# Performance work log

Hardware: AMD Instinct MI355X
Metric: run time of the kernel (lower is better)

## Reference

```python
import jax, jax.numpy as jnp
import numpy as np

B, T, D, H = 256, 512, 128, 64


def _gru_dir(x_tbd, Wi, Wh, bi, bh):
    # PyTorch GRU semantics. x_tbd: [T,B,D]; Wi: [3H,D]; Wh: [3H,H].
    xg = jnp.einsum('tbd,gd->tbg', x_tbd, Wi) + bi  # [T,B,3H]

    def step(h, xg_t):
        hg = h @ Wh.T + bh
        xr, xz, xn = jnp.split(xg_t, 3, axis=-1)
        hr, hz, hn = jnp.split(hg, 3, axis=-1)
        r = jax.nn.sigmoid(xr + hr)
        z = jax.nn.sigmoid(xz + hz)
        n = jnp.tanh(xn + r * hn)
        h = (1.0 - z) * n + z * h
        return h, h

    h0 = jnp.zeros((x_tbd.shape[1], Wh.shape[1]), x_tbd.dtype)
    _, hs = jax.lax.scan(step, h0, xg)
    return hs  # [T,B,H]


def _hb_dir(x_tbd, W, b, U, c):
    # Custom HBLSTM cell. W: [D,5H] (input proj), U: [H,5H] (hidden proj).
    # Gate order: f, i, o, u, k. Both biases folded into the x projection.
    xp = jnp.einsum('tbd,dg->tbg', x_tbd, W) + b + c  # [T,B,5H]

    def step(carry, xp_t):
        h, k, kp = carry
        pre = xp_t + h @ U
        f, i, o, u, kc = jnp.split(pre, 5, axis=-1)
        f = jax.nn.sigmoid(f)
        i = jax.nn.sigmoid(i)
        o = jax.nn.sigmoid(o)
        u = jax.nn.sigmoid(u)
        kp = u * jnp.tanh(kc) + (1.0 - u) * kp
        k = f * k + i * kp
        h = o * jnp.tanh(k)
        return (h, k, kp), h

    z = jnp.zeros((x_tbd.shape[1], U.shape[0]), x_tbd.dtype)
    _, hs = jax.lax.scan(step, (z, z, z), xp)
    return hs  # [T,B,H]


def _forward(x, gru_f_Wi, gru_f_Wh, gru_f_bi, gru_f_bh,
             gru_b_Wi, gru_b_Wh, gru_b_bi, gru_b_bh,
             hb_f_W, hb_f_b, hb_f_U, hb_f_c,
             hb_b_W, hb_b_b, hb_b_U, hb_b_c,
             fast_W, fast_b, stab_W, stab_b,
             attnp_W, attnp_b, attns_W, attns_b,
             gate_W1, gate_b1, gate_W2, gate_b2,
             head_W1, head_b1, head_W2, head_b2):
    xt = jnp.transpose(x, (1, 0, 2))  # [T,B,D]
    xr = xt[::-1]

    # Fast branch: bidirectional GRU; only last-timestep output is used.
    hf = _gru_dir(xt, gru_f_Wi, gru_f_Wh, gru_f_bi, gru_f_bh)
    hb_ = _gru_dir(xr, gru_b_Wi, gru_b_Wh, gru_b_bi, gru_b_bh)
    # fast_seq[:, -1, :] = [fwd hidden at t=T-1, bwd hidden at t=T-1]
    fast_last = jnp.concatenate([hf[-1], hb_[0]], axis=-1) @ fast_W + fast_b

    # Stable branch: bidirectional HBLSTM.
    sf = _hb_dir(xt, hb_f_W, hb_f_b, hb_f_U, hb_f_c)
    sb = _hb_dir(xr, hb_b_W, hb_b_b, hb_b_U, hb_b_c)[::-1]
    stable_seq = jnp.transpose(jnp.concatenate([sf, sb], axis=-1), (1, 0, 2))  # [B,T,2H]

    # Attention pooling over time.
    attn_hidden = jnp.tanh(stable_seq @ attnp_W + attnp_b)        # [B,T,H]
    logits = (attn_hidden @ attns_W + attns_b)[..., 0]            # [B,T]
    w = jax.nn.softmax(logits, axis=1)
    stable_ctx = jnp.einsum('bt,btd->bd', w, stable_seq)
    stable_ctx = stable_ctx @ stab_W + stab_b                     # [B,2H]

    # Gated fusion (dropout is identity in eval).
    g_in = jnp.concatenate([fast_last, stable_ctx], axis=-1)      # [B,4H]
    g_h = jax.nn.relu(g_in @ gate_W1 + gate_b1)
    gate = jax.nn.sigmoid(g_h @ gate_W2 + gate_b2)                # [B,1]
    fused = gate * fast_last + (1.0 - gate) * stable_ctx

    out = jnp.concatenate([fused, fast_last, stable_ctx], axis=-1)  # [B,6H]
    h1 = jax.nn.relu(out @ head_W1 + head_b1)
    return h1 @ head_W2 + head_b2                                  # [B,1]


def setup_inputs() -> dict:
    key = jax.random.key(0)
    ks = iter(jax.random.split(key, 64))

    def p(shape, fan_in):
        return jax.random.normal(next(ks), shape, dtype=jnp.float32) / np.sqrt(fan_in)

    d = {'x': jax.random.normal(next(ks), (B, T, D), dtype=jnp.float32)}
    for pre in ('gru_f', 'gru_b'):
        d[pre + '_Wi'] = p((3 * H, D), D)
        d[pre + '_Wh'] = p((3 * H, H), H)
        d[pre + '_bi'] = p((3 * H,), H)
        d[pre + '_bh'] = p((3 * H,), H)
    for pre in ('hb_f', 'hb_b'):
        d[pre + '_W'] = p((D, 5 * H), D)
        d[pre + '_b'] = p((5 * H,), D)
        d[pre + '_U'] = p((H, 5 * H), H)
        d[pre + '_c'] = p((5 * H,), H)
    d['fast_W'] = p((2 * H, 2 * H), 2 * H); d['fast_b'] = p((2 * H,), 2 * H)
    d['stab_W'] = p((2 * H, 2 * H), 2 * H); d['stab_b'] = p((2 * H,), 2 * H)
    d['attnp_W'] = p((2 * H, H), 2 * H);   d['attnp_b'] = p((H,), 2 * H)
    d['attns_W'] = p((H, 1), H);           d['attns_b'] = p((1,), H)
    d['gate_W1'] = p((4 * H, 2 * H), 4 * H); d['gate_b1'] = p((2 * H,), 4 * H)
    d['gate_W2'] = p((2 * H, 1), 2 * H);     d['gate_b2'] = p((1,), 2 * H)
    d['head_W1'] = p((6 * H, 2 * H), 6 * H); d['head_b1'] = p((2 * H,), 6 * H)
    d['head_W2'] = p((2 * H, 1), 2 * H);     d['head_b2'] = p((1,), 2 * H)
    return d


def reference(x, gru_f_Wi, gru_f_Wh, gru_f_bi, gru_f_bh,
              gru_b_Wi, gru_b_Wh, gru_b_bi, gru_b_bh,
              hb_f_W, hb_f_b, hb_f_U, hb_f_c,
              hb_b_W, hb_b_b, hb_b_U, hb_b_c,
              fast_W, fast_b, stab_W, stab_b,
              attnp_W, attnp_b, attns_W, attns_b,
              gate_W1, gate_b1, gate_W2, gate_b2,
              head_W1, head_b1, head_W2, head_b2):
    return _forward(x, gru_f_Wi, gru_f_Wh, gru_f_bi, gru_f_bh,
                    gru_b_Wi, gru_b_Wh, gru_b_bi, gru_b_bh,
                    hb_f_W, hb_f_b, hb_f_U, hb_f_c,
                    hb_b_W, hb_b_b, hb_b_U, hb_b_c,
                    fast_W, fast_b, stab_W, stab_b,
                    attnp_W, attnp_b, attns_W, attns_b,
                    gate_W1, gate_b1, gate_W2, gate_b2,
                    head_W1, head_b1, head_W2, head_b2)
```

## Files before the change

### kernel.cpp

```cpp
#include <hip/hip_runtime.h>
#include <math.h>

#define B_ 256
#define T_ 512
#define D_ 128
#define H_ 64

static const size_t F_SF    = 0;
static const size_t F_SB    = F_SF + (size_t)T_ * B_ * 64;
static const size_t F_ST    = F_SB + (size_t)T_ * B_ * 64;
static const size_t F_FASTL = F_ST + (size_t)7 * B_ * 64;
static const size_t F_LOG   = F_FASTL + (size_t)B_ * 128;
static const size_t F_CTX   = F_LOG + (size_t)B_ * T_;
static const size_t F_CHUNK = F_CTX + (size_t)B_ * 128;

__device__ __forceinline__ float sigmoidf_(float x) {
    return 1.0f / (1.0f + __expf(-x));
}
__device__ __forceinline__ float tanhf_(float x) {
    float ax = fabsf(x);
    float e  = __expf(-2.0f * ax);
    float t  = (1.0f - e) / (1.0f + e);
    return copysignf(t, x);
}
__device__ __forceinline__ float rl_(float v, int lane) {
    return __int_as_float(__builtin_amdgcn_readlane(__float_as_int(v), lane));
}
__device__ __forceinline__ float wave_sum(float v) {
#pragma unroll
    for (int off = 32; off > 0; off >>= 1) v += __shfl_xor(v, off);
    return v;
}
__device__ __forceinline__ float wave_max(float v) {
#pragma unroll
    for (int off = 32; off > 0; off >>= 1) v = fmaxf(v, __shfl_xor(v, off));
    return v;
}

template<int N, bool WGD, bool REV>
__global__ __launch_bounds__(256) void gemm_in(
    const float* __restrict__ x, const float* __restrict__ W,
    const float* __restrict__ b1, const float* __restrict__ b2,
    float* __restrict__ out, int t0)
{
    __shared__ float a_lds[64 * 68];
    __shared__ float w_lds[64 * 68];

    const int tid = threadIdx.x;
    const int tl  = blockIdx.z;
    const int tg  = t0 + tl;
    const int txi = REV ? (T_ - 1 - tg) : tg;
    const int b0  = blockIdx.y * 64;
    const int g0  = blockIdx.x * 64;

    const int ty = tid >> 4, tx = tid & 15;
    float acc[4][4] = {};

    for (int kh = 0; kh < 2; kh++) {
#pragma unroll
        for (int i = 0; i < 4; i++) {
            int flat = i * 256 + tid;
            int r  = flat >> 4;
            int c4 = flat & 15;
            const float4 v = *reinterpret_cast<const float4*>(
                x + ((size_t)(b0 + r) * T_ + txi) * D_ + kh * 64 + c4 * 4);
            a_lds[(c4 * 4 + 0) * 68 + r] = v.x;
            a_lds[(c4 * 4 + 1) * 68 + r] = v.y;
            a_lds[(c4 * 4 + 2) * 68 + r] = v.z;
            a_lds[(c4 * 4 + 3) * 68 + r] = v.w;
        }
        if (WGD) {
#pragma unroll
            for (int i = 0; i < 4; i++) {
                int flat = i * 256 + tid;
                int r  = flat >> 4;
                int c4 = flat & 15;
                const float4 v = *reinterpret_cast<const float4*>(
                    W + (size_t)(g0 + r) * D_ + kh * 64 + c4 * 4);
                w_lds[(c4 * 4 + 0) * 68 + r] = v.x;
                w_lds[(c4 * 4 + 1) * 68 + r] = v.y;
                w_lds[(c4 * 4 + 2) * 68 + r] = v.z;
                w_lds[(c4 * 4 + 3) * 68 + r] = v.w;
            }
        } else {
#pragma unroll
            for (int i = 0; i < 4; i++) {
                int flat = i * 256 + tid;
                int k  = flat >> 4;
                int c4 = flat & 15;
                const float4 v = *reinterpret_cast<const float4*>(
                    W + (size_t)(kh * 64 + k) * N + g0 + c4 * 4);
                *reinterpret_cast<float4*>(&w_lds[k * 68 + c4 * 4]) = v;
            }
        }
        __syncthreads();
#pragma unroll 8
        for (int k = 0; k < 64; k++) {
            const float4 av = *reinterpret_cast<const float4*>(&a_lds[k * 68 + ty * 4]);
            const float4 wv = *reinterpret_cast<const float4*>(&w_lds[k * 68 + tx * 4]);
            const float am[4] = {av.x, av.y, av.z, av.w};
            const float wn[4] = {wv.x, wv.y, wv.z, wv.w};
#pragma unroll
            for (int mi = 0; mi < 4; mi++)
#pragma unroll
                for (int ni = 0; ni < 4; ni++)
                    acc[mi][ni] = fmaf(am[mi], wn[ni], acc[mi][ni]);
        }
        __syncthreads();
    }

    float bias[4];
#pragma unroll
    for (int ni = 0; ni < 4; ni++) {
        float bb = b1[g0 + tx * 4 + ni];
        if (b2 != nullptr) bb += b2[g0 + tx * 4 + ni];
        bias[ni] = bb;
    }
#pragma unroll
    for (int mi = 0; mi < 4; mi++) {
        float4 o;
        o.x = acc[mi][0] + bias[0];
        o.y = acc[mi][1] + bias[1];
        o.z = acc[mi][2] + bias[2];
        o.w = acc[mi][3] + bias[3];
        *reinterpret_cast<float4*>(
            out + ((size_t)tl * B_ + b0 + ty * 4 + mi) * N + g0 + tx * 4) = o;
    }
}

__global__ __launch_bounds__(256, 1) void recur(
    const float* __restrict__ xg_c, const float* __restrict__ xpf_c,
    const float* __restrict__ xpb_c,
    const float* __restrict__ gWh, const float* __restrict__ gbh,
    const float* __restrict__ Uf,  const float* __restrict__ Ub,
    float* __restrict__ sf, float* __restrict__ sb,
    float* __restrict__ state, int t0, int C)
{
    const int tid   = threadIdx.x;
    const int w     = tid & 63;
    const int wb    = tid >> 6;
    const int chain = blockIdx.x * 4 + wb;

    if (chain < 256) {
        const int batch = chain;
        float* stH = state;
        float h = (t0 == 0) ? 0.0f : stH[(size_t)batch * 64 + w];

        float wh0[64], wh1[64], wh2[64];
#pragma unroll
        for (int j = 0; j < 64; j++) {
            wh0[j] = gWh[(size_t)(0 * 64 + w) * 64 + j];
            wh1[j] = gWh[(size_t)(1 * 64 + w) * 64 + j];
            wh2[j] = gWh[(size_t)(2 * 64 + w) * 64 + j];
            asm volatile("" : "+v"(wh0[j]), "+v"(wh1[j]), "+v"(wh2[j]));
        }
        const float bh0 = gbh[w], bh1 = gbh[64 + w], bh2 = gbh[128 + w];

        float xv0, xv1, xv2;
        {
            const float* p = xg_c + (size_t)batch * 192;
            xv0 = p[w]; xv1 = p[64 + w]; xv2 = p[128 + w];
        }
        for (int t = 0; t < C; t++) {
            float xn0, xn1, xn2;
            {
                int tn = (t + 1 < C) ? (t + 1) : t;
                const float* pn = xg_c + ((size_t)tn * B_ + batch) * 192;
                xn0 = pn[w]; xn1 = pn[64 + w]; xn2 = pn[128 + w];
            }
            float a0 = bh0, a1 = bh1, a2 = bh2;
#pragma unroll
            for (int j = 0; j < 64; j++) {
                const float hj = rl_(h, j);
                a0 = fmaf(hj, wh0[j], a0);
                a1 = fmaf(hj, wh1[j], a1);
                a2 = fmaf(hj, wh2[j], a2);
            }
            float r = sigmoidf_(xv0 + a0);
            float z = sigmoidf_(xv1 + a1);
            float n = tanhf_(xv2 + r * a2);
            h = (1.0f - z) * n + z * h;
            xv0 = xn0; xv1 = xn1; xv2 = xn2;
        }
        stH[(size_t)batch * 64 + w] = h;
    } else {
        const int dir   = (chain >= 512);
        const int batch = chain - (dir ? 512 : 256);
        const float* U  = dir ? Ub : Uf;
        const float* xp = dir ? xpb_c : xpf_c;
        float* outbuf   = dir ? sb : sf;
        float* stH  = state + (size_t)(1 + dir * 3) * B_ * 64;
        float* stK  = stH + (size_t)B_ * 64;
        float* stKp = stK + (size_t)B_ * 64;

        float h, k, kp;
        if (t0 == 0) { h = 0.0f; k = 0.0f; kp = 0.0f; }
        else {
            h  = stH [(size_t)batch * 64 + w];
            k  = stK [(size_t)batch * 64 + w];
            kp = stKp[(size_t)batch * 64 + w];
        }

        float u0[64], u1[64], u2[64], u3[64], u4[64];
#pragma unroll
        for (int j = 0; j < 64; j++) {
            const float* Uj = U + (size_t)j * 320 + w;
            u0[j] = Uj[0];
            u1[j] = Uj[64];
            u2[j] = Uj[128];
            u3[j] = Uj[192];
            u4[j] = Uj[256];
            asm volatile("" : "+v"(u0[j]), "+v"(u1[j]), "+v"(u2[j]),
                              "+v"(u3[j]), "+v"(u4[j]));
        }

        float xv0, xv1, xv2, xv3, xv4;
        {
            const float* p = xp + (size_t)batch * 320;
            xv0 = p[w]; xv1 = p[64 + w]; xv2 = p[128 + w];
            xv3 = p[192 + w]; xv4 = p[256 + w];
        }
        for (int t = 0; t < C; t++) {
            float xn0, xn1, xn2, xn3, xn4;
            {
                int tn = (t + 1 < C) ? (t + 1) : t;
                const float* pn = xp + ((size_t)tn * B_ + batch) * 320;
                xn0 = pn[w]; xn1 = pn[64 + w]; xn2 = pn[128 + w];
                xn3 = pn[192 + w]; xn4 = pn[256 + w];
            }
            float a0 = 0.f, a1 = 0.f, a2 = 0.f, a3 = 0.f, a4 = 0.f;
#pragma unroll
            for (int j = 0; j < 64; j++) {
                const float hj = rl_(h, j);
                a0 = fmaf(hj, u0[j], a0);
                a1 = fmaf(hj, u1[j], a1);
                a2 = fmaf(hj, u2[j], a2);
                a3 = fmaf(hj, u3[j], a3);
                a4 = fmaf(hj, u4[j], a4);
            }
            float f   = sigmoidf_(xv0 + a0);
            float ii  = sigmoidf_(xv1 + a1);
            float o   = sigmoidf_(xv2 + a2);
            float uu  = sigmoidf_(xv3 + a3);
            float tkc = tanhf_(xv4 + a4);
            kp = uu * tkc + (1.0f - uu) * kp;
            k  = f * k + ii * kp;
            h  = o * tanhf_(k);
            int tg   = t0 + t;
            int tout = dir ? (T_ - 1 - tg) : tg;
            outbuf[((size_t)tout * B_ + batch) * 64 + w] = h;
            xv0 = xn0; xv1 = xn1; xv2 = xn2; xv3 = xn3; xv4 = xn4;
        }
        stH [(size_t)batch * 64 + w] = h;
        stK [(size_t)batch * 64 + w] = k;
        stKp[(size_t)batch * 64 + w] = kp;
    }
}

__global__ __launch_bounds__(64) void tail1(
    const float* __restrict__ x, const float* __restrict__ Wib,
    const float* __restrict__ bib, const float* __restrict__ bhb,
    const float* __restrict__ hfl, const float* __restrict__ fW,
    const float* __restrict__ fb, float* __restrict__ fastl)
{
    __shared__ float xrow[128];
    __shared__ float inb[128];
    const int b = blockIdx.x;
    const int l = threadIdx.x;
    xrow[l]      = x[((size_t)b * T_ + (T_ - 1)) * D_ + l];
    xrow[64 + l] = x[((size_t)b * T_ + (T_ - 1)) * D_ + 64 + l];
    inb[l] = hfl[(size_t)b * 64 + l];
    __syncthreads();
    float a0 = bib[l], a1 = bib[64 + l], a2 = bib[128 + l];
#pragma unroll 8
    for (int d = 0; d < 128; d++) {
        float xd = xrow[d];
        a0 = fmaf(xd, Wib[(size_t)l * 128 + d], a0);
        a1 = fmaf(xd, Wib[(size_t)(64 + l) * 128 + d], a1);
        a2 = fmaf(xd, Wib[(size_t)(128 + l) * 128 + d], a2);
    }
    float r = sigmoidf_(a0 + bhb[l]);
    float z = sigmoidf_(a1 + bhb[64 + l]);
    float n = tanhf_(a2 + r * bhb[128 + l]);
    inb[64 + l] = (1.0f - z) * n;
    __syncthreads();
    float acc0 = fb[l], acc1 = fb[64 + l];
#pragma unroll 8
    for (int i2 = 0; i2 < 128; i2++) {
        float v = inb[i2];
        acc0 = fmaf(v, fW[(size_t)i2 * 128 + l], acc0);
        acc1 = fmaf(v, fW[(size_t)i2 * 128 + 64 + l], acc1);
    }
    fastl[(size_t)b * 128 + l]      = acc0;
    fastl[(size_t)b * 128 + 64 + l] = acc1;
}

__global__ __launch_bounds__(256) void attn_logits(
    const float* __restrict__ sf, const float* __restrict__ sb,
    const float* __restrict__ Wp, const float* __restrict__ bp,
    const float* __restrict__ Ws, const float* __restrict__ bs,
    float* __restrict__ logits)
{
    __shared__ float wp_t[64 * 129];
    __shared__ float s_lds[4][132];
    __shared__ float bp_l[64], ws_l[64];
    const int tid = threadIdx.x;
#pragma unroll
    for (int i = 0; i < 32; i++) {
        int idx = i * 256 + tid;
        int d = idx >> 6, g = idx & 63;
        wp_t[g * 129 + d] = Wp[idx];
    }
    if (tid < 64) { bp_l[tid] = bp[tid]; ws_l[tid] = Ws[tid]; }
    __syncthreads();
    const int wave = tid >> 6, l = tid & 63;
    for (int it = 0; it < 64; it++) {
        int p  = blockIdx.x * 256 + wave * 64 + it;
        int bb = p >> 9;
        int t  = p & 511;
        s_lds[wave][l]      = sf[((size_t)t * B_ + bb) * 64 + l];
        s_lds[wave][64 + l] = sb[((size_t)t * B_ + bb) * 64 + l];
        float acc = bp_l[l];
#pragma unroll 8
        for (int d = 0; d < 128; d++)
            acc = fmaf(s_lds[wave][d], wp_t[l * 129 + d], acc);
        float v = tanhf_(acc) * ws_l[l];
        v = wave_sum(v);
        if (l == 0) logits[(size_t)bb * T_ + t] = v + bs[0];
    }
}

__global__ __launch_bounds__(256) void softmax_k(float* __restrict__ logits)
{
    __shared__ float red[8];
    const int b = blockIdx.x, tid = threadIdx.x;
    const int wave = tid >> 6, l = tid & 63;
    float* row = logits + (size_t)b * T_;
    float l0 = row[tid], l1 = row[tid + 256];
    float m = wave_max(fmaxf(l0, l1));
    if (l == 0) red[wave] = m;
    __syncthreads();
    m = fmaxf(fmaxf(red[0], red[1]), fmaxf(red[2], red[3]));
    float e0 = __expf(l0 - m), e1 = __expf(l1 - m);
    float s = wave_sum(e0 + e1);
    if (l == 0) red[4 + wave] = s;
    __syncthreads();
    s = red[4] + red[5] + red[6] + red[7];
    row[tid]       = e0 / s;
    row[tid + 256] = e1 / s;
}

__global__ __launch_bounds__(128) void ctx_k(
    const float* __restrict__ wsm, const float* __restrict__ sf,
    const float* __restrict__ sb, const float* __restrict__ stW,
    const float* __restrict__ stb, float* __restrict__ ctxo)
{
    __shared__ float wrow[512];
    __shared__ float cpre[128];
    const int b = blockIdx.x, tid = threadIdx.x;
#pragma unroll
    for (int i = 0; i < 4; i++) wrow[i * 128 + tid] = wsm[(size_t)b * T_ + i * 128 + tid];
    __syncthreads();
    const float* src = (tid < 64) ? sf : sb;
    const int d = tid & 63;
    float acc = 0.0f;
#pragma unroll 4
    for (int t = 0; t < 512; t++)
        acc = fmaf(wrow[t], src[((size_t)t * B_ + b) * 64 + d], acc);
    cpre[tid] = acc;
    __syncthreads();
    float a2 = stb[tid];
#pragma unroll 8
    for (int i2 = 0; i2 < 128; i2++)
        a2 = fmaf(cpre[i2], stW[(size_t)i2 * 128 + tid], a2);
    ctxo[(size_t)b * 128 + tid] = a2;
}

__global__ __launch_bounds__(128) void tail2(
    const float* __restrict__ fastl, const float* __restrict__ ctxo,
    const float* __restrict__ gW1, const float* __restrict__ gb1,
    const float* __restrict__ gW2, const float* __restrict__ gb2,
    const float* __restrict__ hW1, const float* __restrict__ hb1,
    const float* __restrict__ hW2, const float* __restrict__ hb2,
    float* __restrict__ outp)
{
    __shared__ float gin[256];
    __shared__ float outv[384];
    __shared__ float red2[2];
    const int b = blockIdx.x, tid = threadIdx.x;
    gin[tid]       = fastl[(size_t)b * 128 + tid];
    gin[128 + tid] = ctxo[(size_t)b * 128 + tid];
    __syncthreads();
    float a = gb1[tid];
#pragma unroll 8
    for (int i = 0; i < 256; i++)
        a = fmaf(gin[i], gW1[(size_t)i * 128 + tid], a);
    float gh = fmaxf(a, 0.0f);
    float v = wave_sum(gh * gW2[tid]);
    if ((tid & 63) == 0) red2[tid >> 6] = v;
    __syncthreads();
    float gate = sigmoidf_(red2[0] + red2[1] + gb2[0]);
    float fl = gin[tid], sc = gin[128 + tid];
    outv[tid]       = gate * fl + (1.0f - gate) * sc;
    outv[128 + tid] = fl;
    outv[256 + tid] = sc;
    __syncthreads();
    float a1 = hb1[tid];
#pragma unroll 8
    for (int i = 0; i < 384; i++)
        a1 = fmaf(outv[i], hW1[(size_t)i * 128 + tid], a1);
    float h1v = fmaxf(a1, 0.0f);
    float vv = wave_sum(h1v * hW2[tid]);
    if ((tid & 63) == 0) red2[tid >> 6] = vv;
    __syncthreads();
    if (tid == 0) outp[b] = red2[0] + red2[1] + hb2[0];
}

extern "C" void kernel_launch(void* const* d_in, const int* in_sizes, int n_in,
                              void* d_out, int out_size, void* d_ws, size_t ws_size,
                              hipStream_t stream)
{
    (void)in_sizes; (void)n_in; (void)out_size;
    const float* x      = (const float*)d_in[0];
    const float* gfWi   = (const float*)d_in[1];
    const float* gfWh   = (const float*)d_in[2];
    const float* gfbi   = (const float*)d_in[3];
    const float* gfbh   = (const float*)d_in[4];
    const float* gbWi   = (const float*)d_in[5];
    const float* gbbi   = (const float*)d_in[7];
    const float* gbbh   = (const float*)d_in[8];
    const float* hbfW   = (const float*)d_in[9];
    const float* hbfb   = (const float*)d_in[10];
    const float* hbfU   = (const float*)d_in[11];
    const float* hbfc   = (const float*)d_in[12];
    const float* hbbW   = (const float*)d_in[13];
    const float* hbbb   = (const float*)d_in[14];
    const float* hbbU   = (const float*)d_in[15];
    const float* hbbc   = (const float*)d_in[16];
    const float* fastW  = (const float*)d_in[17];
    const float* fastb  = (const float*)d_in[18];
    const float* stabW  = (const float*)d_in[19];
    const float* stabb  = (const float*)d_in[20];
    const float* attnpW = (const float*)d_in[21];
    const float* attnpb = (const float*)d_in[22];
    const float* attnsW = (const float*)d_in[23];
    const float* attnsb = (const float*)d_in[24];
    const float* gW1    = (const float*)d_in[25];
    const float* gb1    = (const float*)d_in[26];
    const float* gW2    = (const float*)d_in[27];
    const float* gb2    = (const float*)d_in[28];
    const float* hW1    = (const float*)d_in[29];
    const float* hb1    = (const float*)d_in[30];
    const float* hW2    = (const float*)d_in[31];
    const float* hb2    = (const float*)d_in[32];

    float* ws    = (float*)d_ws;
    float* sf    = ws + F_SF;
    float* sb    = ws + F_SB;
    float* st    = ws + F_ST;
    float* fastl = ws + F_FASTL;
    float* logit = ws + F_LOG;
    float* ctxo  = ws + F_CTX;

    const size_t wsf = ws_size / sizeof(float);
    int C = T_;
    while (C > 1 && F_CHUNK + (size_t)C * B_ * 832 > wsf) C >>= 1;
    const int nc = T_ / C;

    float* xg_c  = ws + F_CHUNK;
    float* xpf_c = xg_c  + (size_t)C * B_ * 192;
    float* xpb_c = xpf_c + (size_t)C * B_ * 320;

    for (int c = 0; c < nc; c++) {
        const int t0 = c * C;
        gemm_in<192, true,  false><<<dim3(3, 4, C), 256, 0, stream>>>(x, gfWi, gfbi, nullptr, xg_c, t0);
        gemm_in<320, false, false><<<dim3(5, 4, C), 256, 0, stream>>>(x, hbfW, hbfb, hbfc, xpf_c, t0);
        gemm_in<320, false, true ><<<dim3(5, 4, C), 256, 0, stream>>>(x, hbbW, hbbb, hbbc, xpb_c, t0);
        recur<<<dim3(192), 256, 0, stream>>>(xg_c, xpf_c, xpb_c, gfWh, gfbh, hbfU, hbbU,
                                             sf, sb, st, t0, C);
    }

    tail1<<<dim3(B_), 64, 0, stream>>>(x, gbWi, gbbi, gbbh, st, fastW, fastb, fastl);

    attn_logits<<<dim3(512), 256, 0, stream>>>(sf, sb, attnpW, attnpb, attnsW, attnsb, logit);
    softmax_k<<<dim3(B_), 256, 0, stream>>>(logit);
    ctx_k<<<dim3(B_), 128, 0, stream>>>(logit, sf, sb, stabW, stabb, ctxo);

    tail2<<<dim3(B_), 128, 0, stream>>>(fastl, ctxo, gW1, gb1, gW2, gb2,
                                        hW1, hb1, hW2, hb2, (float*)d_out);
}
```

Baseline: 1.598 ms.

## Split recurrent matvec across two waves per chain and enlarge input GEMM tiles

The recurrent kernel now splits each chain's hidden-state matvec across two wavefronts. Each wave holds half of the recurrent weights and exchanges partial sums through double-buffered LDS with a block barrier every timestep. This halves the serial FMA chain per step and the register pressure, at the cost of a __syncthreads per timestep that couples the chains sharing a block. Separately, the input-projection GEMM tile grows to 128 batch rows with 8x4 accumulators per thread and XOR-swizzled LDS addressing to reduce bank conflicts.

```diff
diff --git a/kernel.cpp b/kernel.cpp
--- a/kernel.cpp
+++ b/kernel.cpp
@@ -37,71 +37,110 @@
     return v;
 }
 
+template<int BASE>
+__device__ __forceinline__ void hb_acc(float h,
+    const float* u0, const float* u1, const float* u2,
+    const float* u3, const float* u4,
+    float& a0, float& a1, float& a2, float& a3, float& a4)
+{
+#pragma unroll
+    for (int jj = 0; jj < 32; jj++) {
+        const float hj = rl_(h, BASE + jj);
+        a0 = fmaf(hj, u0[jj], a0);
+        a1 = fmaf(hj, u1[jj], a1);
+        a2 = fmaf(hj, u2[jj], a2);
+        a3 = fmaf(hj, u3[jj], a3);
+        a4 = fmaf(hj, u4[jj], a4);
+    }
+}
+template<int BASE>
+__device__ __forceinline__ void gru_acc(float h,
+    const float* w0, const float* w1, const float* w2,
+    float& a0, float& a1, float& a2)
+{
+#pragma unroll
+    for (int jj = 0; jj < 32; jj++) {
+        const float hj = rl_(h, BASE + jj);
+        a0 = fmaf(hj, w0[jj], a0);
+        a1 = fmaf(hj, w1[jj], a1);
+        a2 = fmaf(hj, w2[jj], a2);
+    }
+}
+
 template<int N, bool WGD, bool REV>
-__global__ __launch_bounds__(256) void gemm_in(
+__global__ __launch_bounds__(256, 1) void gemm_in(
     const float* __restrict__ x, const float* __restrict__ W,
     const float* __restrict__ b1, const float* __restrict__ b2,
     float* __restrict__ out, int t0)
 {
-    __shared__ float a_lds[64 * 68];
+    __shared__ float a_lds[64 * 132];
     __shared__ float w_lds[64 * 68];
 
     const int tid = threadIdx.x;
     const int tl  = blockIdx.z;
     const int tg  = t0 + tl;
     const int txi = REV ? (T_ - 1 - tg) : tg;
-    const int b0  = blockIdx.y * 64;
+    const int b0  = blockIdx.y * 128;
     const int g0  = blockIdx.x * 64;
 
     const int ty = tid >> 4, tx = tid & 15;
-    float acc[4][4] = {};
+    float acc[8][4] = {};
 
     for (int kh = 0; kh < 2; kh++) {
 #pragma unroll
-        for (int i = 0; i < 4; i++) {
+        for (int i = 0; i < 8; i++) {
             int flat = i * 256 + tid;
-            int r  = flat >> 4;
-            int c4 = flat & 15;
+            int r    = flat >> 4;
+            int c4   = flat & 15;
             const float4 v = *reinterpret_cast<const float4*>(
                 x + ((size_t)(b0 + r) * T_ + txi) * D_ + kh * 64 + c4 * 4);
-            a_lds[(c4 * 4 + 0) * 68 + r] = v.x;
-            a_lds[(c4 * 4 + 1) * 68 + r] = v.y;
-            a_lds[(c4 * 4 + 2) * 68 + r] = v.z;
-            a_lds[(c4 * 4 + 3) * 68 + r] = v.w;
+            const int rs = r ^ ((c4 & 7) << 2);
+            a_lds[(c4 * 4 + 0) * 132 + rs] = v.x;
+            a_lds[(c4 * 4 + 1) * 132 + rs] = v.y;
+            a_lds[(c4 * 4 + 2) * 132 + rs] = v.z;
+            a_lds[(c4 * 4 + 3) * 132 + rs] = v.w;
         }
         if (WGD) {
 #pragma unroll
             for (int i = 0; i < 4; i++) {
                 int flat = i * 256 + tid;
-                int r  = flat >> 4;
-                int c4 = flat & 15;
+                int r    = flat >> 4;
+                int c4   = flat & 15;
                 const float4 v = *reinterpret_cast<const float4*>(
                     W + (size_t)(g0 + r) * D_ + kh * 64 + c4 * 4);
-                w_lds[(c4 * 4 + 0) * 68 + r] = v.x;
-                w_lds[(c4 * 4 + 1) * 68 + r] = v.y;
-                w_lds[(c4 * 4 + 2) * 68 + r] = v.z;
-                w_lds[(c4 * 4 + 3) * 68 + r] = v.w;
+                const int rs = r ^ ((c4 & 7) << 2);
+                w_lds[(c4 * 4 + 0) * 68 + rs] = v.x;
+                w_lds[(c4 * 4 + 1) * 68 + rs] = v.y;
+                w_lds[(c4 * 4 + 2) * 68 + rs] = v.z;
+                w_lds[(c4 * 4 + 3) * 68 + rs] = v.w;
             }
         } else {
 #pragma unroll
             for (int i = 0; i < 4; i++) {
                 int flat = i * 256 + tid;
-                int k  = flat >> 4;
-                int c4 = flat & 15;
+                int k    = flat >> 4;
+                int c4   = flat & 15;
                 const float4 v = *reinterpret_cast<const float4*>(
                     W + (size_t)(kh * 64 + k) * N + g0 + c4 * 4);
-                *reinterpret_cast<float4*>(&w_lds[k * 68 + c4 * 4]) = v;
+                const int ns = (c4 * 4) ^ (((k >> 2) & 7) << 2);
+                *reinterpret_cast<float4*>(&w_lds[k * 68 + ns]) = v;
             }
         }
         __syncthreads();
 #pragma unroll 8
         for (int k = 0; k < 64; k++) {
-            const float4 av = *reinterpret_cast<const float4*>(&a_lds[k * 68 + ty * 4]);
-            const float4 wv = *reinterpret_cast<const float4*>(&w_lds[k * 68 + tx * 4]);
-            const float am[4] = {av.x, av.y, av.z, av.w};
-            const float wn[4] = {wv.x, wv.y, wv.z, wv.w};
-#pragma unroll
-            for (int mi = 0; mi < 4; mi++)
+            const int sw = ((k >> 2) & 7) << 2;
+            const float4 am0 = *reinterpret_cast<const float4*>(
+                &a_lds[k * 132 + ((ty * 8) ^ sw)]);
+            const float4 am1 = *reinterpret_cast<const float4*>(
+                &a_lds[k * 132 + ((ty * 8 + 4) ^ sw)]);
+            const float4 wn4 = *reinterpret_cast<const float4*>(
+                &w_lds[k * 68 + ((tx * 4) ^ sw)]);
+            const float am[8] = {am0.x, am0.y, am0.z, am0.w,
+                                 am1.x, am1.y, am1.z, am1.w};
+            const float wn[4] = {wn4.x, wn4.y, wn4.z, wn4.w};
+#pragma unroll
+            for (int mi = 0; mi < 8; mi++)
 #pragma unroll
                 for (int ni = 0; ni < 4; ni++)
                     acc[mi][ni] = fmaf(am[mi], wn[ni], acc[mi][ni]);
@@ -117,18 +156,18 @@
         bias[ni] = bb;
     }
 #pragma unroll
-    for (int mi = 0; mi < 4; mi++) {
+    for (int mi = 0; mi < 8; mi++) {
         float4 o;
         o.x = acc[mi][0] + bias[0];
         o.y = acc[mi][1] + bias[1];
         o.z = acc[mi][2] + bias[2];
         o.w = acc[mi][3] + bias[3];
         *reinterpret_cast<float4*>(
-            out + ((size_t)tl * B_ + b0 + ty * 4 + mi) * N + g0 + tx * 4) = o;
-    }
-}
-
-__global__ __launch_bounds__(256, 1) void recur(
+            out + ((size_t)tl * B_ + b0 + ty * 8 + mi) * N + g0 + tx * 4) = o;
+    }
+}
+
+__global__ __launch_bounds__(384, 1) void recur(
     const float* __restrict__ xg_c, const float* __restrict__ xpf_c,
     const float* __restrict__ xpb_c,
     const float* __restrict__ gWh, const float* __restrict__ gbh,
@@ -136,56 +175,18 @@
     float* __restrict__ sf, float* __restrict__ sb,
     float* __restrict__ state, int t0, int C)
 {
-    const int tid   = threadIdx.x;
-    const int w     = tid & 63;
-    const int wb    = tid >> 6;
-    const int chain = blockIdx.x * 4 + wb;
-
-    if (chain < 256) {
-        const int batch = chain;
-        float* stH = state;
-        float h = (t0 == 0) ? 0.0f : stH[(size_t)batch * 64 + w];
-
-        float wh0[64], wh1[64], wh2[64];
-#pragma unroll
-        for (int j = 0; j < 64; j++) {
-            wh0[j] = gWh[(size_t)(0 * 64 + w) * 64 + j];
-            wh1[j] = gWh[(size_t)(1 * 64 + w) * 64 + j];
-            wh2[j] = gWh[(size_t)(2 * 64 + w) * 64 + j];
-            asm volatile("" : "+v"(wh0[j]), "+v"(wh1[j]), "+v"(wh2[j]));
-        }
-        const float bh0 = gbh[w], bh1 = gbh[64 + w], bh2 = gbh[128 + w];
-
-        float xv0, xv1, xv2;
-        {
-            const float* p = xg_c + (size_t)batch * 192;
-            xv0 = p[w]; xv1 = p[64 + w]; xv2 = p[128 + w];
-        }
-        for (int t = 0; t < C; t++) {
-            float xn0, xn1, xn2;
-            {
-                int tn = (t + 1 < C) ? (t + 1) : t;
-                const float* pn = xg_c + ((size_t)tn * B_ + batch) * 192;
-                xn0 = pn[w]; xn1 = pn[64 + w]; xn2 = pn[128 + w];
-            }
-            float a0 = bh0, a1 = bh1, a2 = bh2;
-#pragma unroll
-            for (int j = 0; j < 64; j++) {
-                const float hj = rl_(h, j);
-                a0 = fmaf(hj, wh0[j], a0);
-                a1 = fmaf(hj, wh1[j], a1);
-                a2 = fmaf(hj, wh2[j], a2);
-            }
-            float r = sigmoidf_(xv0 + a0);
-            float z = sigmoidf_(xv1 + a1);
-            float n = tanhf_(xv2 + r * a2);
-            h = (1.0f - z) * n + z * h;
-            xv0 = xn0; xv1 = xn1; xv2 = xn2;
-        }
-        stH[(size_t)batch * 64 + w] = h;
-    } else {
-        const int dir   = (chain >= 512);
-        const int batch = chain - (dir ? 512 : 256);
+    __shared__ float hpart[2][2][2][5][64];
+    __shared__ float gpart[2][2][3][64];
+    const int tid = threadIdx.x;
+    const int w   = tid & 63;
+    const int wv  = tid >> 6;
+
+    if (wv < 4) {
+        const int lc    = wv >> 1;
+        const int p     = wv & 1;
+        const int hb    = blockIdx.x * 2 + lc;
+        const int dir   = hb >= 256 ? 1 : 0;
+        const int batch = hb - (dir ? 256 : 0);
         const float* U  = dir ? Ub : Uf;
         const float* xp = dir ? xpb_c : xpf_c;
         float* outbuf   = dir ? sb : sf;
@@ -201,24 +202,24 @@
             kp = stKp[(size_t)batch * 64 + w];
         }
 
-        float u0[64], u1[64], u2[64], u3[64], u4[64];
-#pragma unroll
-        for (int j = 0; j < 64; j++) {
-            const float* Uj = U + (size_t)j * 320 + w;
-            u0[j] = Uj[0];
-            u1[j] = Uj[64];
-            u2[j] = Uj[128];
-            u3[j] = Uj[192];
-            u4[j] = Uj[256];
-            asm volatile("" : "+v"(u0[j]), "+v"(u1[j]), "+v"(u2[j]),
-                              "+v"(u3[j]), "+v"(u4[j]));
+        float u0[32], u1[32], u2[32], u3[32], u4[32];
+#pragma unroll
+        for (int jj = 0; jj < 32; jj++) {
+            const float* Uj = U + (size_t)(p * 32 + jj) * 320 + w;
+            u0[jj] = Uj[0];
+            u1[jj] = Uj[64];
+            u2[jj] = Uj[128];
+            u3[jj] = Uj[192];
+            u4[jj] = Uj[256];
+            asm volatile("" : "+v"(u0[jj]), "+v"(u1[jj]), "+v"(u2[jj]),
+                              "+v"(u3[jj]), "+v"(u4[jj]));
         }
 
         float xv0, xv1, xv2, xv3, xv4;
         {
-            const float* p = xp + (size_t)batch * 320;
-            xv0 = p[w]; xv1 = p[64 + w]; xv2 = p[128 + w];
-            xv3 = p[192 + w]; xv4 = p[256 + w];
+            const float* pp = xp + (size_t)batch * 320;
+            xv0 = pp[w]; xv1 = pp[64 + w]; xv2 = pp[128 + w];
+            xv3 = pp[192 + w]; xv4 = pp[256 + w];
         }
         for (int t = 0; t < C; t++) {
             float xn0, xn1, xn2, xn3, xn4;
@@ -229,15 +230,22 @@
                 xn3 = pn[192 + w]; xn4 = pn[256 + w];
             }
             float a0 = 0.f, a1 = 0.f, a2 = 0.f, a3 = 0.f, a4 = 0.f;
-#pragma unroll
-            for (int j = 0; j < 64; j++) {
-                const float hj = rl_(h, j);
-                a0 = fmaf(hj, u0[j], a0);
-                a1 = fmaf(hj, u1[j], a1);
-                a2 = fmaf(hj, u2[j], a2);
-                a3 = fmaf(hj, u3[j], a3);
-                a4 = fmaf(hj, u4[j], a4);
-            }
+            if (p == 0) hb_acc<0 >(h, u0, u1, u2, u3, u4, a0, a1, a2, a3, a4);
+            else        hb_acc<32>(h, u0, u1, u2, u3, u4, a0, a1, a2, a3, a4);
+
+            const int bf = t & 1;
+            hpart[bf][lc][p][0][w] = a0;
+            hpart[bf][lc][p][1][w] = a1;
+            hpart[bf][lc][p][2][w] = a2;
+            hpart[bf][lc][p][3][w] = a3;
+            hpart[bf][lc][p][4][w] = a4;
+            __syncthreads();
+            a0 += hpart[bf][lc][1 - p][0][w];
+            a1 += hpart[bf][lc][1 - p][1][w];
+            a2 += hpart[bf][lc][1 - p][2][w];
+            a3 += hpart[bf][lc][1 - p][3][w];
+            a4 += hpart[bf][lc][1 - p][4][w];
+
             float f   = sigmoidf_(xv0 + a0);
             float ii  = sigmoidf_(xv1 + a1);
             float o   = sigmoidf_(xv2 + a2);
@@ -246,14 +254,67 @@
             kp = uu * tkc + (1.0f - uu) * kp;
             k  = f * k + ii * kp;
             h  = o * tanhf_(k);
-            int tg   = t0 + t;
-            int tout = dir ? (T_ - 1 - tg) : tg;
-            outbuf[((size_t)tout * B_ + batch) * 64 + w] = h;
+            if (p == 0) {
+                int tg   = t0 + t;
+                int tout = dir ? (T_ - 1 - tg) : tg;
+                outbuf[((size_t)tout * B_ + batch) * 64 + w] = h;
+            }
             xv0 = xn0; xv1 = xn1; xv2 = xn2; xv3 = xn3; xv4 = xn4;
         }
-        stH [(size_t)batch * 64 + w] = h;
-        stK [(size_t)batch * 64 + w] = k;
-        stKp[(size_t)batch * 64 + w] = kp;
+        if (p == 0) {
+            stH [(size_t)batch * 64 + w] = h;
+            stK [(size_t)batch * 64 + w] = k;
+            stKp[(size_t)batch * 64 + w] = kp;
+        }
+    } else {
+        const int p     = wv - 4;
+        const int batch = blockIdx.x;
+        float* stH = state;
+        float h = (t0 == 0) ? 0.0f : stH[(size_t)batch * 64 + w];
+
+        float wh0[32], wh1[32], wh2[32];
+#pragma unroll
+        for (int jj = 0; jj < 32; jj++) {
+            const int j = p * 32 + jj;
+            wh0[jj] = gWh[(size_t)(0 * 64 + w) * 64 + j];
+            wh1[jj] = gWh[(size_t)(1 * 64 + w) * 64 + j];
+            wh2[jj] = gWh[(size_t)(2 * 64 + w) * 64 + j];
+            asm volatile("" : "+v"(wh0[jj]), "+v"(wh1[jj]), "+v"(wh2[jj]));
+        }
+        const float bh0 = gbh[w], bh1 = gbh[64 + w], bh2 = gbh[128 + w];
+
+        float xv0, xv1, xv2;
+        {
+            const float* pp = xg_c + (size_t)batch * 192;
+            xv0 = pp[w]; xv1 = pp[64 + w]; xv2 = pp[128 + w];
+        }
+        for (int t = 0; t < C; t++) {
+            float xn0, xn1, xn2;
+            {
+                int tn = (t + 1 < C) ? (t + 1) : t;
+                const float* pn = xg_c + ((size_t)tn * B_ + batch) * 192;
+                xn0 = pn[w]; xn1 = pn[64 + w]; xn2 = pn[128 + w];
+            }
+            float a0 = 0.f, a1 = 0.f, a2 = 0.f;
+            if (p == 0) gru_acc<0 >(h, wh0, wh1, wh2, a0, a1, a2);
+            else        gru_acc<32>(h, wh0, wh1, wh2, a0, a1, a2);
+
+            const int bf = t & 1;
+            gpart[bf][p][0][w] = a0;
+            gpart[bf][p][1][w] = a1;
+            gpart[bf][p][2][w] = a2;
+            __syncthreads();
+            a0 += gpart[bf][1 - p][0][w];
+            a1 += gpart[bf][1 - p][1][w];
+            a2 += gpart[bf][1 - p][2][w];
+
+            float r = sigmoidf_(xv0 + bh0 + a0);
+            float z = sigmoidf_(xv1 + bh1 + a1);
+            float n = tanhf_(xv2 + r * (bh2 + a2));
+            h = (1.0f - z) * n + z * h;
+            xv0 = xn0; xv1 = xn1; xv2 = xn2;
+        }
+        if (p == 0) stH[(size_t)batch * 64 + w] = h;
     }
 }
 
@@ -473,10 +534,10 @@
 
     for (int c = 0; c < nc; c++) {
         const int t0 = c * C;
-        gemm_in<192, true,  false><<<dim3(3, 4, C), 256, 0, stream>>>(x, gfWi, gfbi, nullptr, xg_c, t0);
-        gemm_in<320, false, false><<<dim3(5, 4, C), 256, 0, stream>>>(x, hbfW, hbfb, hbfc, xpf_c, t0);
-        gemm_in<320, false, true ><<<dim3(5, 4, C), 256, 0, stream>>>(x, hbbW, hbbb, hbbc, xpb_c, t0);
-        recur<<<dim3(192), 256, 0, stream>>>(xg_c, xpf_c, xpb_c, gfWh, gfbh, hbfU, hbbU,
+        gemm_in<192, true,  false><<<dim3(3, 2, C), 256, 0, stream>>>(x, gfWi, gfbi, nullptr, xg_c, t0);
+        gemm_in<320, false, false><<<dim3(5, 2, C), 256, 0, stream>>>(x, hbfW, hbfb, hbfc, xpf_c, t0);
+        gemm_in<320, false, true ><<<dim3(5, 2, C), 256, 0, stream>>>(x, hbbW, hbbb, hbbc, xpb_c, t0);
+        recur<<<dim3(256), 384, 0, stream>>>(xg_c, xpf_c, xpb_c, gfWh, gfbh, hbfU, hbbU,
                                              sf, sb, st, t0, C);
     }
 
```

Result: faster. 1.313 ms (-17.8%).
